# Optimization experiments

Measured on AMD Instinct MI355X. Metric: run time of the kernel, lower is better.

## Reference

```python
import jax, jax.numpy as jnp
import numpy as np
from jax import lax

ROUTING_ITERS = 3
CLASSES = 10
CAPS_DIM = 8
N_CAPS = 32 * 6 * 6  # 1152
DN = ('NCHW', 'OIHW', 'NCHW')


def setup_inputs() -> dict:
    key = jax.random.key(0)
    k1, k2, k3, k4 = jax.random.split(key, 4)
    x = jax.random.normal(k1, (256, 1, 28, 28), dtype=jnp.float32)
    conv1_w = jax.random.normal(k2, (256, 1, 9, 9), dtype=jnp.float32) * 0.05
    conv1_b = jnp.zeros((256,), dtype=jnp.float32)
    conv2_w = jax.random.normal(k3, (256, 256, 9, 9), dtype=jnp.float32) * 0.01
    conv2_b = jnp.zeros((256,), dtype=jnp.float32)
    # torch.randn init, as in the original Parameter
    W = jax.random.normal(k4, (CLASSES, N_CAPS, 16, CAPS_DIM), dtype=jnp.float32)
    return {"x": x, "conv1_w": conv1_w, "conv1_b": conv1_b,
            "conv2_w": conv2_w, "conv2_b": conv2_b, "W": W}


def _squash_primary(t):
    # module-level squash: scale = norm^2/(1+norm^2), NO division by norm
    sq = jnp.sum(t * t, axis=-1, keepdims=True)
    return (sq / (1.0 + sq)) * t


def _squash_routing(t):
    # CapsNet.squash: scale = sq/(1+sq) * t / sqrt(sq)
    sq = jnp.sum(t * t, axis=-1, keepdims=True)
    return (sq / (1.0 + sq)) * t / jnp.sqrt(sq)


def reference(x, conv1_w, conv1_b, conv2_w, conv2_b, W):
    B = x.shape[0]
    h = lax.conv_general_dilated(x, conv1_w, (1, 1), 'VALID', dimension_numbers=DN)
    h = h + conv1_b[None, :, None, None]
    h = jax.nn.relu(h)                    # [B,256,20,20]
    h = lax.conv_general_dilated(h, conv2_w, (2, 2), 'VALID', dimension_numbers=DN)
    h = h + conv2_b[None, :, None, None]  # [B,256,6,6]
    u = h.reshape(B, -1, CAPS_DIM)        # [B,1152,8]
    u = _squash_primary(u)
    xp = jnp.transpose(u, (1, 2, 0))      # [1152,8,B]
    # broadcasted matmul: [C,1152,16,8] @ [1152,8,B] -> [C,1152,16,B]
    u_hat = jnp.einsum('cnij,njb->cnib', W, xp)
    b = jnp.zeros_like(u_hat)
    outputs = None
    for i in range(ROUTING_ITERS):
        probs = jax.nn.softmax(b, axis=1)               # over the 1152 capsules
        s = jnp.sum(probs * u_hat, axis=1, keepdims=True)  # [C,1,16,B]
        outputs = _squash_routing(s)                    # squash over last (batch) axis
        if i != ROUTING_ITERS - 1:
            delta_b = jnp.sum(u_hat * outputs, axis=-1, keepdims=True)
            b = b + delta_b
    out = jnp.squeeze(outputs, axis=1)    # [C,16,B]
    out = jnp.transpose(out, (2, 0, 1))   # [B,C,16]
    return jnp.sum(out * out, axis=2)     # [B,C]
```

## Files before the change

kernel.cpp:

```cpp
#include <hip/hip_runtime.h>
#include <math.h>

using short8 = __attribute__((ext_vector_type(8))) short;
using f32x16 = __attribute__((ext_vector_type(16))) float;

static const size_t B_QHI = 0;
static const size_t B_QLO = 47316992;
static const size_t B_WHI = 94633984;
static const size_t B_WLO = 105250816;
static const size_t B_H2  = 115867648;
static const size_t B_END = 125304832;
static const size_t B_UH  = 0;
static const size_t B_OB  = 94633984;

__device__ __forceinline__ unsigned short bf16_rne(float v) {
    unsigned int u = __builtin_bit_cast(unsigned int, v);
    u += 0x7FFFu + ((u >> 16) & 1u);
    return (unsigned short)(u >> 16);
}
__device__ __forceinline__ float bf16_tof(unsigned short h) {
    unsigned int u = ((unsigned int)h) << 16;
    return __builtin_bit_cast(float, u);
}

__global__ __launch_bounds__(256) void conv1_kernel(
        const float* __restrict__ x, const float* __restrict__ w1,
        const float* __restrict__ b1,
        unsigned short* __restrict__ qhi, unsigned short* __restrict__ qlo) {
    int b  = blockIdx.x;
    int xh = blockIdx.y;
    int c  = threadIdx.x;
    __shared__ float xs[28][20];
    for (int i = c; i < 560; i += 256) {
        int row = i / 20, cl = i - row * 20, gc = xh * 10 + cl;
        xs[row][cl] = (gc < 28) ? x[(size_t)b*784 + row*28 + gc] : 0.f;
    }
    float wr[81];
    #pragma unroll
    for (int k = 0; k < 81; ++k) wr[k] = w1[c*81 + k];
    float bias = b1[c];
    __syncthreads();
    for (int oy = 0; oy < 19; ++oy) {
        float acc[12];
        #pragma unroll
        for (int e = 0; e < 12; ++e) acc[e] = 0.f;
        #pragma unroll
        for (int ky = 0; ky < 9; ++ky) {
            float xr[20];
            #pragma unroll
            for (int i = 0; i < 20; ++i) xr[i] = xs[oy + ky][i];
            #pragma unroll
            for (int kx = 0; kx < 9; ++kx) {
                float wv_ = wr[ky*9 + kx];
                #pragma unroll
                for (int e = 0; e < 12; ++e)
                    acc[e] = fmaf(xr[e + kx], wv_, acc[e]);
            }
        }
        #pragma unroll
        for (int e = 0; e < 12; ++e) {
            int ox = xh*10 + e;
            if (e < 10 && ox < 19) {
                float v = fmaxf(bias + acc[e], 0.f);
                unsigned short hi = bf16_rne(v);
                unsigned short lo = bf16_rne(v - bf16_tof(hi));
                size_t o = ((size_t)((oy*19 + ox)*16 + (c >> 4))*256 + b)*16 + (c & 15);
                qhi[o] = hi; qlo[o] = lo;
            }
        }
    }
}

__global__ __launch_bounds__(256) void w2t_kernel(
        const float* __restrict__ w2,
        unsigned short* __restrict__ whi, unsigned short* __restrict__ wlo) {
    int c    = blockIdx.x;
    int half = blockIdx.y;
    int t = threadIdx.x;
    __shared__ float buf[128*81];
    const float* src = w2 + (size_t)c*20736 + (size_t)half*128*81;
    for (int i = t; i < 128*81; i += 256) buf[i] = src[i];
    __syncthreads();
    int kk = t >> 7, cil = t & 127;
    int ci = half*128 + cil;
    size_t cbase = ((size_t)(c >> 5)*16 + (ci >> 4))*32 + (c & 31);
    for (int k2 = 0; k2 < 41; ++k2) {
        int k = k2*2 + kk;
        if (k < 81) {
            float v = buf[cil*81 + k];
            unsigned short hi = bf16_rne(v);
            unsigned short lo = bf16_rne(v - bf16_tof(hi));
            size_t o = (((size_t)k*4096 + cbase)*16) + (ci & 15);
            whi[o] = hi; wlo[o] = lo;
        }
    }
}

__global__ __launch_bounds__(512) void conv2_mfma(
        const unsigned short* __restrict__ qhi, const unsigned short* __restrict__ qlo,
        const unsigned short* __restrict__ whi, const unsigned short* __restrict__ wlo,
        const float* __restrict__ b2, float* __restrict__ h2t) {
    int blk = blockIdx.x;
    int bt  = blk & 7;
    int rest = blk >> 3;
    int cg = rest & 7;
    int oyx = rest >> 3;
    int oxh = oyx & 1, oy = oyx >> 1;
    int qx0 = oxh * 6;
    int t = threadIdx.x;
    int wv = t >> 6, l = t & 63;

    int loff = (l & 31)*16 + (l >> 5)*8;

    f32x16 acc[3];
    #pragma unroll
    for (int i = 0; i < 3; ++i)
        #pragma unroll
        for (int r = 0; r < 16; ++r) acc[i][r] = 0.f;

    #pragma unroll 1
    for (int ky = 0; ky < 9; ++ky) {
        int qy = oy*2 + ky;
        #pragma unroll 1
        for (int cc = 0; cc < 2; ++cc) {
            int cis = wv*2 + cc;
            short8 afh[13], afl[13], bfh[9], bfl[9];
            size_t abase = (((size_t)(qy*19 + qx0)*16 + cis)*256)*16 + (size_t)bt*512 + loff;
            #pragma unroll
            for (int q = 0; q < 13; ++q) {
                afh[q] = *(const short8*)(qhi + abase + (size_t)q*65536);
                afl[q] = *(const short8*)(qlo + abase + (size_t)q*65536);
            }
            size_t bbase = (((size_t)(ky*9)*8 + cg)*16 + cis)*512 + loff;
            #pragma unroll
            for (int kx = 0; kx < 9; ++kx) {
                bfh[kx] = *(const short8*)(whi + bbase + (size_t)kx*65536);
                bfl[kx] = *(const short8*)(wlo + bbase + (size_t)kx*65536);
            }
            #pragma unroll
            for (int kx = 0; kx < 9; ++kx) {
                #pragma unroll
                for (int oxl = 0; oxl < 3; ++oxl) {
                    int q = 2*oxl + kx;
                    acc[oxl] = __builtin_amdgcn_mfma_f32_32x32x16_bf16(afh[q], bfh[kx], acc[oxl], 0, 0, 0);
                    acc[oxl] = __builtin_amdgcn_mfma_f32_32x32x16_bf16(afh[q], bfl[kx], acc[oxl], 0, 0, 0);
                    acc[oxl] = __builtin_amdgcn_mfma_f32_32x32x16_bf16(afl[q], bfh[kx], acc[oxl], 0, 0, 0);
                }
            }
        }
    }

    __shared__ float buf[4][3][16][64];
    if (wv < 4) {
        #pragma unroll
        for (int i = 0; i < 3; ++i)
            #pragma unroll
            for (int r = 0; r < 16; ++r)
                buf[wv][i][r][l] = acc[i][r];
    }
    __syncthreads();
    if (wv >= 4) {
        #pragma unroll
        for (int i = 0; i < 3; ++i)
            #pragma unroll
            for (int r = 0; r < 16; ++r)
                buf[wv-4][i][r][l] += acc[i][r];
    }
    __syncthreads();

    float* ebuf = &buf[0][0][0][0];
    if (wv == 0) {
        float bv = b2[cg*32 + (l & 31)];
        float vals[3][16];
        #pragma unroll
        for (int i = 0; i < 3; ++i)
            #pragma unroll
            for (int r = 0; r < 16; ++r)
                vals[i][r] = buf[0][i][r][l] + buf[1][i][r][l]
                           + buf[2][i][r][l] + buf[3][i][r][l] + bv;
        #pragma unroll
        for (int i = 0; i < 3; ++i)
            #pragma unroll
            for (int r = 0; r < 16; ++r) {
                int row = (r & 3) + 8*(r >> 2) + 4*(l >> 5);
                ebuf[i*1056 + row*33 + (l & 31)] = vals[i][r];
            }
    }
    __syncthreads();
    #pragma unroll 1
    for (int pass = 0; pass < 6; ++pass) {
        int row_id = pass*16 + (t >> 5);
        int oxl = row_id >> 5, c = row_id & 31;
        float v = ebuf[oxl*1056 + (t & 31)*33 + c];
        int p = oy*6 + oxh*3 + oxl;
        h2t[(size_t)((cg*32 + c)*36 + p)*256 + bt*32 + (t & 31)] = v;
    }
}

__global__ __launch_bounds__(256) void uhat_kernel(
        const float* __restrict__ h2t, const float* __restrict__ W,
        unsigned short* __restrict__ uhat) {
    int ch = blockIdx.x;
    int c  = blockIdx.y;
    int t  = threadIdx.x;
    __shared__ float Wl[2048];
    const float* wsrc = W + ((size_t)c*1152 + ch*16)*128;
    for (int i = t; i < 2048; i += 256) Wl[i] = wsrc[i];
    __syncthreads();
    #pragma unroll 1
    for (int nn = 0; nn < 16; ++nn) {
        int n = ch*16 + nn;
        float v[8]; float sq = 0.f;
        #pragma unroll
        for (int j = 0; j < 8; ++j) {
            v[j] = h2t[(size_t)(n*8 + j)*256 + t];
            sq = fmaf(v[j], v[j], sq);
        }
        float sc = sq / (1.0f + sq);
        #pragma unroll
        for (int j = 0; j < 8; ++j) v[j] *= sc;
        #pragma unroll
        for (int i = 0; i < 16; ++i) {
            float uh = 0.f;
            #pragma unroll
            for (int j = 0; j < 8; ++j)
                uh = fmaf(Wl[(nn*16 + i)*8 + j], v[j], uh);
            uhat[((size_t)(c*16 + i)*1152 + n)*256 + t] = bf16_rne(uh);
        }
    }
}

__global__ __launch_bounds__(512) void rout_kernel(
        const unsigned short* __restrict__ uhat, float* __restrict__ ob) {
    int ci = blockIdx.x;
    int t  = threadIdx.x;
    int wv = t >> 6, l = t & 63;
    const unsigned short* U = uhat + (size_t)ci*1152*256;
    __shared__ float bsum[1152];
    __shared__ float p[1152];
    __shared__ float outb[256];
    __shared__ float sred[16][256];
    __shared__ float red[8];
    for (int k = t; k < 1152; k += 512) bsum[k] = 0.f;
    __syncthreads();

    #pragma unroll 1
    for (int it = 0; it < 3; ++it) {
        float lv[3];
        float m = -1e30f;
        #pragma unroll
        for (int k = 0; k < 3; ++k) {
            int n = t + k*512;
            lv[k] = (n < 1152) ? bsum[n] : -1e30f;
            m = fmaxf(m, lv[k]);
        }
        #pragma unroll
        for (int mm = 1; mm < 64; mm <<= 1) m = fmaxf(m, __shfl_xor(m, mm, 64));
        if (l == 0) red[wv] = m;
        __syncthreads();
        m = red[0];
        #pragma unroll
        for (int k = 1; k < 8; ++k) m = fmaxf(m, red[k]);
        __syncthreads();
        float se = 0.f;
        #pragma unroll
        for (int k = 0; k < 3; ++k) {
            int n = t + k*512;
            if (n < 1152) {
                float e = expf(lv[k] - m);
                p[n] = e;
                se += e;
            }
        }
        #pragma unroll
        for (int mm = 1; mm < 64; mm <<= 1) se += __shfl_xor(se, mm, 64);
        if (l == 0) red[wv] = se;
        __syncthreads();
        se = red[0];
        #pragma unroll
        for (int k = 1; k < 8; ++k) se += red[k];
        float inv = 1.0f / se;
        #pragma unroll
        for (int k = 0; k < 3; ++k) {
            int n = t + k*512;
            if (n < 1152) p[n] *= inv;
        }
        __syncthreads();

        {
            int ng = t >> 5, bo = t & 31;
            float s8[8];
            #pragma unroll
            for (int e = 0; e < 8; ++e) s8[e] = 0.f;
            int n0 = ng * 72;
            #pragma unroll 4
            for (int nn = 0; nn < 72; ++nn) {
                int n = n0 + nn;
                float pv = p[n];
                short8 u8 = *(const short8*)(U + (size_t)n*256 + bo*8);
                #pragma unroll
                for (int e = 0; e < 8; ++e)
                    s8[e] = fmaf(pv, bf16_tof((unsigned short)u8[e]), s8[e]);
            }
            #pragma unroll
            for (int e = 0; e < 8; ++e) sred[ng][bo*8 + e] = s8[e];
        }
        __syncthreads();

        float s = 0.f;
        if (t < 256) {
            #pragma unroll
            for (int g = 0; g < 16; ++g) s += sred[g][t];
            float v2 = s * s;
            #pragma unroll
            for (int mm = 1; mm < 64; mm <<= 1) v2 += __shfl_xor(v2, mm, 64);
            if ((t & 63) == 0) red[t >> 6] = v2;
        }
        __syncthreads();
        float total = red[0] + red[1] + red[2] + red[3];
        if (t < 256) {
            float scq = total / ((1.0f + total) * sqrtf(total));
            float o = scq * s;
            if (it == 2) ob[(size_t)ci*256 + t] = o;
            else outb[t] = o;
        }
        if (it == 2) break;
        __syncthreads();

        {
            int nl = l >> 5, bo = l & 31;
            #pragma unroll 2
            for (int pass = 0; pass < 72; ++pass) {
                int n = pass*16 + wv*2 + nl;
                short8 u8 = *(const short8*)(U + (size_t)n*256 + bo*8);
                float d = 0.f;
                #pragma unroll
                for (int e = 0; e < 8; ++e)
                    d = fmaf(bf16_tof((unsigned short)u8[e]), outb[bo*8 + e], d);
                #pragma unroll
                for (int mm = 1; mm < 32; mm <<= 1) d += __shfl_xor(d, mm, 64);
                if (bo == 0) bsum[n] += d;
            }
        }
        __syncthreads();
    }
}

__global__ __launch_bounds__(256) void final_kernel(
        const float* __restrict__ obuf, float* __restrict__ out) {
    int c = blockIdx.x;
    int t = threadIdx.x;
    float s = 0.0f;
    #pragma unroll
    for (int i = 0; i < 16; ++i) {
        float v = obuf[((size_t)c*16 + i)*256 + t];
        s = fmaf(v, v, s);
    }
    out[(size_t)t*10 + c] = s;
}

extern "C" void kernel_launch(void* const* d_in, const int* in_sizes, int n_in,
                              void* d_out, int out_size, void* d_ws, size_t ws_size,
                              hipStream_t stream) {
    const float* x  = (const float*)d_in[0];
    const float* w1 = (const float*)d_in[1];
    const float* b1 = (const float*)d_in[2];
    const float* w2 = (const float*)d_in[3];
    const float* b2 = (const float*)d_in[4];
    const float* W  = (const float*)d_in[5];
    float* out = (float*)d_out;
    (void)in_sizes; (void)n_in; (void)out_size;

    if (ws_size < B_END) return;

    char* wsb = (char*)d_ws;
    unsigned short* qhi = (unsigned short*)(wsb + B_QHI);
    unsigned short* qlo = (unsigned short*)(wsb + B_QLO);
    unsigned short* whi = (unsigned short*)(wsb + B_WHI);
    unsigned short* wlo = (unsigned short*)(wsb + B_WLO);
    float* h2t = (float*)(wsb + B_H2);
    unsigned short* uh = (unsigned short*)(wsb + B_UH);
    float* ob = (float*)(wsb + B_OB);

    w2t_kernel<<<dim3(256, 2), 256, 0, stream>>>(w2, whi, wlo);
    conv1_kernel<<<dim3(256, 2), 256, 0, stream>>>(x, w1, b1, qhi, qlo);
    conv2_mfma<<<768, 512, 0, stream>>>(qhi, qlo, whi, wlo, b2, h2t);
    uhat_kernel<<<dim3(72, 10), 256, 0, stream>>>(h2t, W, uh);
    rout_kernel<<<160, 512, 0, stream>>>(uh, ob);
    final_kernel<<<10, 256, 0, stream>>>(ob, out);
}
```

Baseline: 538.3 us.

## Compute two output-channel groups per conv2 block to reuse A fragments

Each conv2 MFMA block now computes two 32-channel output groups, reusing the loaded input (A) fragments for both, and the grid is halved from 768 to 384 blocks. This halves global reads of the split-bf16 activations. In exchange it doubles the accumulator and B-fragment registers, which may lower occupancy or cause spills. With 384 blocks the grid is close to the CU count, so it may also leave the GPU underfilled.

```diff
diff --git a/kernel.cpp b/kernel.cpp
--- a/kernel.cpp
+++ b/kernel.cpp
@@ -103,8 +103,8 @@
     int blk = blockIdx.x;
     int bt  = blk & 7;
     int rest = blk >> 3;
-    int cg = rest & 7;
-    int oyx = rest >> 3;
+    int cgp = rest & 3;
+    int oyx = rest >> 2;
     int oxh = oyx & 1, oy = oyx >> 1;
     int qx0 = oxh * 6;
     int t = threadIdx.x;
@@ -112,11 +112,11 @@
 
     int loff = (l & 31)*16 + (l >> 5)*8;
 
-    f32x16 acc[3];
+    f32x16 acc0[3], acc1[3];
     #pragma unroll
     for (int i = 0; i < 3; ++i)
         #pragma unroll
-        for (int r = 0; r < 16; ++r) acc[i][r] = 0.f;
+        for (int r = 0; r < 16; ++r) { acc0[i][r] = 0.f; acc1[i][r] = 0.f; }
 
     #pragma unroll 1
     for (int ky = 0; ky < 9; ++ky) {
@@ -124,77 +124,86 @@
         #pragma unroll 1
         for (int cc = 0; cc < 2; ++cc) {
             int cis = wv*2 + cc;
-            short8 afh[13], afl[13], bfh[9], bfl[9];
+            short8 afh[13], afl[13], b0h[9], b0l[9], b1h[9], b1l[9];
             size_t abase = (((size_t)(qy*19 + qx0)*16 + cis)*256)*16 + (size_t)bt*512 + loff;
             #pragma unroll
             for (int q = 0; q < 13; ++q) {
                 afh[q] = *(const short8*)(qhi + abase + (size_t)q*65536);
                 afl[q] = *(const short8*)(qlo + abase + (size_t)q*65536);
             }
-            size_t bbase = (((size_t)(ky*9)*8 + cg)*16 + cis)*512 + loff;
+            size_t bbase = (((size_t)(ky*9)*8 + cgp*2)*16 + cis)*512 + loff;
             #pragma unroll
             for (int kx = 0; kx < 9; ++kx) {
-                bfh[kx] = *(const short8*)(whi + bbase + (size_t)kx*65536);
-                bfl[kx] = *(const short8*)(wlo + bbase + (size_t)kx*65536);
+                b0h[kx] = *(const short8*)(whi + bbase + (size_t)kx*65536);
+                b0l[kx] = *(const short8*)(wlo + bbase + (size_t)kx*65536);
+                b1h[kx] = *(const short8*)(whi + bbase + 8192 + (size_t)kx*65536);
+                b1l[kx] = *(const short8*)(wlo + bbase + 8192 + (size_t)kx*65536);
             }
             #pragma unroll
             for (int kx = 0; kx < 9; ++kx) {
                 #pragma unroll
                 for (int oxl = 0; oxl < 3; ++oxl) {
                     int q = 2*oxl + kx;
-                    acc[oxl] = __builtin_amdgcn_mfma_f32_32x32x16_bf16(afh[q], bfh[kx], acc[oxl], 0, 0, 0);
-                    acc[oxl] = __builtin_amdgcn_mfma_f32_32x32x16_bf16(afh[q], bfl[kx], acc[oxl], 0, 0, 0);
-                    acc[oxl] = __builtin_amdgcn_mfma_f32_32x32x16_bf16(afl[q], bfh[kx], acc[oxl], 0, 0, 0);
+                    acc0[oxl] = __builtin_amdgcn_mfma_f32_32x32x16_bf16(afh[q], b0h[kx], acc0[oxl], 0, 0, 0);
+                    acc0[oxl] = __builtin_amdgcn_mfma_f32_32x32x16_bf16(afh[q], b0l[kx], acc0[oxl], 0, 0, 0);
+                    acc0[oxl] = __builtin_amdgcn_mfma_f32_32x32x16_bf16(afl[q], b0h[kx], acc0[oxl], 0, 0, 0);
+                    acc1[oxl] = __builtin_amdgcn_mfma_f32_32x32x16_bf16(afh[q], b1h[kx], acc1[oxl], 0, 0, 0);
+                    acc1[oxl] = __builtin_amdgcn_mfma_f32_32x32x16_bf16(afh[q], b1l[kx], acc1[oxl], 0, 0, 0);
+                    acc1[oxl] = __builtin_amdgcn_mfma_f32_32x32x16_bf16(afl[q], b1h[kx], acc1[oxl], 0, 0, 0);
                 }
             }
         }
     }
 
     __shared__ float buf[4][3][16][64];
-    if (wv < 4) {
-        #pragma unroll
-        for (int i = 0; i < 3; ++i)
-            #pragma unroll
-            for (int r = 0; r < 16; ++r)
-                buf[wv][i][r][l] = acc[i][r];
-    }
-    __syncthreads();
-    if (wv >= 4) {
-        #pragma unroll
-        for (int i = 0; i < 3; ++i)
-            #pragma unroll
-            for (int r = 0; r < 16; ++r)
-                buf[wv-4][i][r][l] += acc[i][r];
-    }
-    __syncthreads();
-
-    float* ebuf = &buf[0][0][0][0];
-    if (wv == 0) {
-        float bv = b2[cg*32 + (l & 31)];
-        float vals[3][16];
-        #pragma unroll
-        for (int i = 0; i < 3; ++i)
-            #pragma unroll
-            for (int r = 0; r < 16; ++r)
-                vals[i][r] = buf[0][i][r][l] + buf[1][i][r][l]
-                           + buf[2][i][r][l] + buf[3][i][r][l] + bv;
-        #pragma unroll
-        for (int i = 0; i < 3; ++i)
-            #pragma unroll
-            for (int r = 0; r < 16; ++r) {
-                int row = (r & 3) + 8*(r >> 2) + 4*(l >> 5);
-                ebuf[i*1056 + row*33 + (l & 31)] = vals[i][r];
-            }
-    }
-    __syncthreads();
-    #pragma unroll 1
-    for (int pass = 0; pass < 6; ++pass) {
-        int row_id = pass*16 + (t >> 5);
-        int oxl = row_id >> 5, c = row_id & 31;
-        float v = ebuf[oxl*1056 + (t & 31)*33 + c];
-        int p = oy*6 + oxh*3 + oxl;
-        h2t[(size_t)((cg*32 + c)*36 + p)*256 + bt*32 + (t & 31)] = v;
-    }
+    #define REDUCE_STORE(ACC, CGL)                                              \
+    {                                                                           \
+        if (wv < 4) {                                                           \
+            _Pragma("unroll")                                                   \
+            for (int i = 0; i < 3; ++i)                                         \
+                _Pragma("unroll")                                               \
+                for (int r = 0; r < 16; ++r) buf[wv][i][r][l] = ACC[i][r];      \
+        }                                                                       \
+        __syncthreads();                                                        \
+        if (wv >= 4) {                                                          \
+            _Pragma("unroll")                                                   \
+            for (int i = 0; i < 3; ++i)                                         \
+                _Pragma("unroll")                                               \
+                for (int r = 0; r < 16; ++r) buf[wv-4][i][r][l] += ACC[i][r];   \
+        }                                                                       \
+        __syncthreads();                                                        \
+        float* ebuf = &buf[0][0][0][0];                                         \
+        if (wv == 0) {                                                          \
+            float bv = b2[(cgp*2 + (CGL))*32 + (l & 31)];                       \
+            float vals[3][16];                                                  \
+            _Pragma("unroll")                                                   \
+            for (int i = 0; i < 3; ++i)                                         \
+                _Pragma("unroll")                                               \
+                for (int r = 0; r < 16; ++r)                                    \
+                    vals[i][r] = buf[0][i][r][l] + buf[1][i][r][l]              \
+                               + buf[2][i][r][l] + buf[3][i][r][l] + bv;        \
+            _Pragma("unroll")                                                   \
+            for (int i = 0; i < 3; ++i)                                         \
+                _Pragma("unroll")                                               \
+                for (int r = 0; r < 16; ++r) {                                  \
+                    int row = (r & 3) + 8*(r >> 2) + 4*(l >> 5);                \
+                    ebuf[i*1056 + row*33 + (l & 31)] = vals[i][r];              \
+                }                                                               \
+        }                                                                       \
+        __syncthreads();                                                        \
+        _Pragma("unroll 1")                                                     \
+        for (int pass = 0; pass < 6; ++pass) {                                  \
+            int row_id = pass*16 + (t >> 5);                                    \
+            int oxl = row_id >> 5, c = row_id & 31;                             \
+            float v = ebuf[oxl*1056 + (t & 31)*33 + c];                         \
+            int p = oy*6 + oxh*3 + oxl;                                         \
+            h2t[(size_t)(((cgp*2 + (CGL))*32 + c)*36 + p)*256 + bt*32 + (t & 31)] = v; \
+        }                                                                       \
+        __syncthreads();                                                        \
+    }
+    REDUCE_STORE(acc0, 0)
+    REDUCE_STORE(acc1, 1)
+    #undef REDUCE_STORE
 }
 
 __global__ __launch_bounds__(256) void uhat_kernel(
@@ -384,7 +393,7 @@
 
     w2t_kernel<<<dim3(256, 2), 256, 0, stream>>>(w2, whi, wlo);
     conv1_kernel<<<dim3(256, 2), 256, 0, stream>>>(x, w1, b1, qhi, qlo);
-    conv2_mfma<<<768, 512, 0, stream>>>(qhi, qlo, whi, wlo, b2, h2t);
+    conv2_mfma<<<384, 512, 0, stream>>>(qhi, qlo, whi, wlo, b2, h2t);
     uhat_kernel<<<dim3(72, 10), 256, 0, stream>>>(h2t, W, uh);
     rout_kernel<<<160, 512, 0, stream>>>(uh, ob);
     final_kernel<<<10, 256, 0, stream>>>(ob, out);
```

Result: slower. 615.1 us (+14.3%).
